# Performance work log

Measured on AMD Instinct MI355X. Metric: run time of the kernel, lower is better.

## Reference

```python
import jax, jax.numpy as jnp
import numpy as np

B, S, D_MODEL, D_ATTN = 4, 2048, 1024, 1024
NEG_INF = jnp.float32(-jnp.inf)


def setup_inputs() -> dict:
    key = jax.random.key(0)
    ks = jax.random.split(key, 6)
    scale = 1.0 / np.sqrt(D_MODEL)
    return {
        "x": jax.random.normal(ks[0], (B, S, D_MODEL), dtype=jnp.float32),
        "mask": jnp.ones((B, S), dtype=jnp.float32),
        "Wq": jax.random.normal(ks[1], (D_ATTN, D_MODEL), dtype=jnp.float32) * scale,
        "Wk": jax.random.normal(ks[2], (D_ATTN, D_MODEL), dtype=jnp.float32) * scale,
        "Wv": jax.random.normal(ks[3], (D_ATTN, D_MODEL), dtype=jnp.float32) * scale,
        "Wo": jax.random.normal(ks[4], (D_MODEL, D_ATTN), dtype=jnp.float32) * scale,
        "bo": jnp.zeros((D_MODEL,), dtype=jnp.float32),
    }


def reference(x, mask, Wq, Wk, Wv, Wo, bo):
    # x: [B,S,Dm]; torch Linear weight is [out,in], so y = x @ W.T
    q = jnp.einsum("bsd,ad->bsa", x, Wq)  # [B,S,Da]
    k = jnp.einsum("bsd,ad->bsa", x, Wk)
    v = jnp.einsum("bsd,ad->bsa", x, Wv)  # NOTE: v from x (original quirk)
    logits = jnp.einsum("bqa,bka->bqk", q, k)  # [B,S,S]
    # causal mask (cross_attention=True path): keep lower triangle incl. diag
    causal = jnp.tril(jnp.ones((S, S), dtype=bool))
    logits = jnp.where(causal[None], logits, NEG_INF)
    # padding mask: outer product of per-token mask
    square_mask = mask[:, :, None] * mask[:, None, :]  # [B,S,S]
    logits = jnp.where(square_mask == 1, logits, NEG_INF)
    # scale by sqrt(d_model) AFTER masking (as in original)
    attn = jax.nn.softmax(logits / jnp.sqrt(jnp.float32(D_MODEL)), axis=-1)
    attn_out = jnp.einsum("bqk,bka->bqa", attn, v)  # [B,S,Da]
    return jnp.einsum("bsa,da->bsd", attn_out, Wo) + bo
```

## Files before the change

### kernel.cpp

```cpp
#include <hip/hip_runtime.h>
#include <hip/hip_bf16.h>
#include <cstdio>

typedef __bf16 bf16x8 __attribute__((ext_vector_type(8)));
typedef float f32x4 __attribute__((ext_vector_type(4)));

#define BM 128
#define BN 128
#define BK 64

__device__ __forceinline__ unsigned short f2bf(float f) {
  union { float f; unsigned u; } v; v.f = f;
  unsigned u = v.u;
  return (unsigned short)((u + 0x7FFFu + ((u >> 16) & 1u)) >> 16);
}

__device__ __forceinline__ float bf2f(unsigned short s) {
  union { unsigned u; float f; } v; v.u = ((unsigned)s) << 16;
  return v.f;
}

#define GLOAD16(gsrc, ldst) \
  __builtin_amdgcn_global_load_lds((const __attribute__((address_space(1))) void*)(gsrc), \
                                   (__attribute__((address_space(3))) void*)(ldst), 16, 0, 0)

template<int EPI>
__global__ __launch_bounds__(256, 2)
void gemm_bt(const unsigned short* __restrict__ A, const unsigned short* __restrict__ B,
             void* __restrict__ Cv, void* __restrict__ Cv2, const float* __restrict__ bias,
             int K, int ldA, int ldB, int ldC,
             long aBat, long bBat, long cBat,
             int causalSkip, int causalKlim, float scale, int revM)
{
  const int by = revM ? (gridDim.y - 1 - blockIdx.y) : blockIdx.y;
  const int m0 = by * BM;
  const int n0 = blockIdx.x * BN;
  if (causalSkip && n0 > m0) return;
  const int bz = blockIdx.z;

  const unsigned short* Ab = A + (long)bz * aBat + (long)m0 * ldA;
  const unsigned short* Bb = B + (long)bz * bBat + (long)n0 * ldB;

  __shared__ short lds[2][2][BM * BK];

  const int tid = threadIdx.x;
  const int lane = tid & 63;
  const int wave = tid >> 6;
  const int wr = wave >> 1, wc = wave & 1;

  const int Keff = causalKlim ? min(K, m0 + BM) : K;
  const int nk = Keff / BK;

  const int srow = tid >> 3;
  const int sch = tid & 7;

  const f32x4 fzero = {0.f, 0.f, 0.f, 0.f};
  f32x4 acc[4][4];
#pragma unroll
  for (int i = 0; i < 4; i++)
#pragma unroll
    for (int j = 0; j < 4; j++) acc[i][j] = fzero;

  int aOff[4][2], bOff[4][2];
#pragma unroll
  for (int i = 0; i < 4; i++) {
#pragma unroll
    for (int s = 0; s < 2; s++) {
      int ra = wr * 64 + i * 16 + (lane & 15);
      aOff[i][s] = ra * BK + (((s * 4 + (lane >> 4)) ^ (ra & 7)) * 8);
      int rb = wc * 64 + i * 16 + (lane & 15);
      bOff[i][s] = rb * BK + (((s * 4 + (lane >> 4)) ^ (rb & 7)) * 8);
    }
  }

  auto stage = [&](int buf, int kt) {
    const unsigned short* Ak = Ab + kt * BK;
    const unsigned short* Bk = Bb + kt * BK;
#pragma unroll
    for (int r = 0; r < 4; r++) {
      int row = r * 32 + srow;
      int sc = sch ^ (row & 7);
      GLOAD16(Ak + (long)row * ldA + sc * 8, &lds[buf][0][(r * 32 + wave * 8) * BK]);
    }
#pragma unroll
    for (int r = 0; r < 4; r++) {
      int row = r * 32 + srow;
      int sc = sch ^ (row & 7);
      GLOAD16(Bk + (long)row * ldB + sc * 8, &lds[buf][1][(r * 32 + wave * 8) * BK]);
    }
  };

  stage(0, 0);
  __syncthreads();

  int cur = 0;
  for (int kt = 0; kt < nk; kt++) {
    if (kt + 1 < nk) stage(cur ^ 1, kt + 1);
    const short* La = lds[cur][0];
    const short* Lb = lds[cur][1];
#pragma unroll
    for (int s = 0; s < 2; s++) {
      bf16x8 av[4], bv[4];
#pragma unroll
      for (int i = 0; i < 4; i++) av[i] = *reinterpret_cast<const bf16x8*>(La + aOff[i][s]);
#pragma unroll
      for (int j = 0; j < 4; j++) bv[j] = *reinterpret_cast<const bf16x8*>(Lb + bOff[j][s]);
#pragma unroll
      for (int i = 0; i < 4; i++)
#pragma unroll
        for (int j = 0; j < 4; j++)
          acc[i][j] = __builtin_amdgcn_mfma_f32_16x16x32_bf16(av[i], bv[j], acc[i][j], 0, 0, 0);
    }
    __syncthreads();
    cur ^= 1;
  }

  const int rb4 = (lane >> 4) * 4;
  const int cl = lane & 15;
#pragma unroll
  for (int i = 0; i < 4; i++) {
#pragma unroll
    for (int j = 0; j < 4; j++) {
      const int gm = m0 + wr * 64 + i * 16 + rb4;
      const int gn = n0 + wc * 64 + j * 16 + cl;
      if (EPI == 0) {
        unsigned short* C = (unsigned short*)Cv + (long)bz * cBat;
#pragma unroll
        for (int r = 0; r < 4; r++)
          C[(long)(gm + r) * ldC + gn] = f2bf(acc[i][j][r] * scale);
      } else if (EPI == 2) {
        float* C = (float*)Cv;
        const float bb = bias[gn];
#pragma unroll
        for (int r = 0; r < 4; r++)
          C[(long)(gm + r) * ldC + gn] = acc[i][j][r] + bb;
      } else if (EPI == 4) {
        if (gn < 2048) {
          unsigned short* C = (unsigned short*)Cv;
#pragma unroll
          for (int r = 0; r < 4; r++)
            C[(long)(gm + r) * ldC + gn] = f2bf(acc[i][j][r]);
        } else {
          const int d = gn - 2048;
          const int b = gm >> 11;
          const int sIdx = gm & 2047;
          unsigned short* C = (unsigned short*)Cv2 + (long)b * (2048L * 1024)
                              + (long)d * 2048 + sIdx;
          ushort4 pk;
          pk.x = f2bf(acc[i][j][0]);
          pk.y = f2bf(acc[i][j][1]);
          pk.z = f2bf(acc[i][j][2]);
          pk.w = f2bf(acc[i][j][3]);
          *reinterpret_cast<ushort4*>(C) = pk;
        }
      }
    }
  }
}

__global__ __launch_bounds__(256)
void softmax_rows(const unsigned short* __restrict__ Sb, const float* __restrict__ maskv,
                  unsigned short* __restrict__ P, int Sdim)
{
  const int q = blockIdx.x;
  const int b = blockIdx.y;
  const int kmax = (q & ~127) + 128;
  const unsigned short* row = Sb + ((long)b * Sdim + q) * Sdim;
  unsigned short* prow = P + ((long)b * Sdim + q) * Sdim;
  const float* mrow = maskv + (long)b * Sdim;
  const int tid = threadIdx.x;
  const float mq = mrow[q];
  const int k0 = tid * 8;
  const bool live = (k0 < kmax);

  float v[8];
  if (live) {
    uint4 raw = *reinterpret_cast<const uint4*>(row + k0);
    const unsigned short* us = reinterpret_cast<const unsigned short*>(&raw);
    float4 ma = *reinterpret_cast<const float4*>(mrow + k0);
    float4 mb = *reinterpret_cast<const float4*>(mrow + k0 + 4);
    float mv[8] = {ma.x, ma.y, ma.z, ma.w, mb.x, mb.y, mb.z, mb.w};
#pragma unroll
    for (int u = 0; u < 8; u++) {
      const int k = k0 + u;
      const bool ok = (k <= q) && (mq * mv[u] == 1.0f);
      v[u] = ok ? bf2f(us[u]) : -INFINITY;
    }
  } else {
#pragma unroll
    for (int u = 0; u < 8; u++) v[u] = -INFINITY;
  }

  float mx = -INFINITY;
#pragma unroll
  for (int u = 0; u < 8; u++) mx = fmaxf(mx, v[u]);
#pragma unroll
  for (int o = 32; o; o >>= 1) mx = fmaxf(mx, __shfl_xor(mx, o));
  __shared__ float redm[4], reds[4];
  if ((tid & 63) == 0) redm[tid >> 6] = mx;
  __syncthreads();
  mx = fmaxf(fmaxf(redm[0], redm[1]), fmaxf(redm[2], redm[3]));

  float p[8];
  float sm = 0.f;
#pragma unroll
  for (int u = 0; u < 8; u++) {
    p[u] = (v[u] > -INFINITY) ? __expf(v[u] - mx) : 0.f;
    sm += p[u];
  }
#pragma unroll
  for (int o = 32; o; o >>= 1) sm += __shfl_xor(sm, o);
  if ((tid & 63) == 0) reds[tid >> 6] = sm;
  __syncthreads();
  sm = reds[0] + reds[1] + reds[2] + reds[3];
  const float inv = 1.0f / sm;

  if (live) {
    union { unsigned short us[8]; uint4 u4; } pk;
#pragma unroll
    for (int u = 0; u < 8; u++) pk.us[u] = f2bf(p[u] * inv);
    *reinterpret_cast<uint4*>(prow + k0) = pk.u4;
  }
}

__global__ __launch_bounds__(256)
void cast_f32_bf16(const float* __restrict__ in, unsigned short* __restrict__ out, int n)
{
  const int i = (blockIdx.x * 256 + threadIdx.x) * 8;
  if (i >= n) return;
  float4 a = *reinterpret_cast<const float4*>(in + i);
  float4 b = *reinterpret_cast<const float4*>(in + i + 4);
  union { unsigned short us[8]; uint4 u4; } pk;
  pk.us[0] = f2bf(a.x); pk.us[1] = f2bf(a.y); pk.us[2] = f2bf(a.z); pk.us[3] = f2bf(a.w);
  pk.us[4] = f2bf(b.x); pk.us[5] = f2bf(b.y); pk.us[6] = f2bf(b.z); pk.us[7] = f2bf(b.w);
  *reinterpret_cast<uint4*>(out + i) = pk.u4;
}

__global__ __launch_bounds__(256)
void cast_weights(const float* __restrict__ w0, const float* __restrict__ w1,
                  const float* __restrict__ w2, const float* __restrict__ w3,
                  unsigned short* __restrict__ dqkv, unsigned short* __restrict__ dout)
{
  const int z = blockIdx.z;
  const float* src = (z == 0) ? w0 : (z == 1) ? w1 : (z == 2) ? w2 : w3;
  unsigned short* dst = (z < 3) ? (dqkv + (long)z * 1024 * 1024) : dout;
  const int i = (blockIdx.x * 256 + threadIdx.x) * 8;
  float4 a = *reinterpret_cast<const float4*>(src + i);
  float4 b = *reinterpret_cast<const float4*>(src + i + 4);
  union { unsigned short us[8]; uint4 u4; } pk;
  pk.us[0] = f2bf(a.x); pk.us[1] = f2bf(a.y); pk.us[2] = f2bf(a.z); pk.us[3] = f2bf(a.w);
  pk.us[4] = f2bf(b.x); pk.us[5] = f2bf(b.y); pk.us[6] = f2bf(b.z); pk.us[7] = f2bf(b.w);
  *reinterpret_cast<uint4*>(dst + i) = pk.u4;
}

extern "C" void kernel_launch(void* const* d_in, const int* in_sizes, int n_in,
                              void* d_out, int out_size, void* d_ws, size_t ws_size,
                              hipStream_t stream)
{
  const int B = 4, S = 2048, D = 1024;
  const float* x  = (const float*)d_in[0];
  const float* mk = (const float*)d_in[1];
  const float* Wq = (const float*)d_in[2];
  const float* Wk = (const float*)d_in[3];
  const float* Wv = (const float*)d_in[4];
  const float* Wo = (const float*)d_in[5];
  const float* bo = (const float*)d_in[6];
  float* out = (float*)d_out;

  char* ws = (char*)d_ws;
  const long MB = 1024L * 1024L;
  unsigned short* Xbf  = (unsigned short*)(ws + 0);
  unsigned short* QKb  = (unsigned short*)(ws + 16 * MB);
  unsigned short* Vt   = (unsigned short*)(ws + 48 * MB);
  unsigned short* Wqkv = (unsigned short*)(ws + 64 * MB);
  unsigned short* Wob  = (unsigned short*)(ws + 70 * MB);
  unsigned short* Sbuf = (unsigned short*)(ws + 72 * MB);
  unsigned short* P    = QKb;
  unsigned short* O    = Xbf;

  if (ws_size < (size_t)(104 * MB)) {
    fprintf(stderr, "kernel_launch: ws too small (%zu bytes, need 104MB)\n", ws_size);
    return;
  }

  cast_f32_bf16<<<dim3((B * S * D) / 8 / 256), 256, 0, stream>>>(x, Xbf, B * S * D);
  cast_weights<<<dim3((D * D) / 8 / 256, 1, 4), 256, 0, stream>>>(Wq, Wk, Wv, Wo, Wqkv, Wob);

  const dim3 blk(256);
  dim3 gQKV(3072 / BN, 8192 / BM, 1);
  gemm_bt<4><<<gQKV, blk, 0, stream>>>(Xbf, Wqkv, QKb, Vt, nullptr,
                                       1024, 1024, 1024, 2048,
                                       0, 0, 0, 0, 0, 1.0f, 0);
  dim3 gS(2048 / BN, 2048 / BM, 4);
  gemm_bt<0><<<gS, blk, 0, stream>>>(QKb, QKb + 1024, Sbuf, nullptr, nullptr,
                                     1024, 2048, 2048, 2048,
                                     (long)S * 2048, (long)S * 2048, (long)S * S,
                                     1, 0, 0.03125f, 0);
  softmax_rows<<<dim3(2048, 4), blk, 0, stream>>>(Sbuf, mk, P, 2048);
  dim3 gO(1024 / BN, 2048 / BM, 4);
  gemm_bt<0><<<gO, blk, 0, stream>>>(P, Vt, O, nullptr, nullptr,
                                     2048, 2048, 2048, 1024,
                                     (long)S * S, (long)D * S, (long)S * D,
                                     0, 1, 1.0f, 1);
  dim3 gF(1024 / BN, 8192 / BM, 1);
  gemm_bt<2><<<gF, blk, 0, stream>>>(O, Wob, out, nullptr, bo,
                                     1024, 1024, 1024, 1024,
                                     0, 0, 0, 0, 0, 1.0f, 0);
}
```

Measured before the change: 185.9 us.

## Single-buffer GEMM LDS, raise occupancy, add XCD block swizzle, split Q/K outputs

The GEMM now uses a single LDS buffer instead of double buffering, which halves shared memory, and raises the launch-bounds occupancy hint from 2 to 3 blocks. Block indices are remapped so that consecutive tiles land on the same XCD for better L2 reuse. Q and K are written to separate contiguous buffers instead of one interleaved one, and the two cast kernels are merged into one launch. The cost is that global loads are no longer overlapped with MFMA work within a block, so latency hiding now relies on more resident blocks.

After: 183.0 us. About the same (-1.6%).

```diff
diff --git a/kernel.cpp b/kernel.cpp
--- a/kernel.cpp
+++ b/kernel.cpp
@@ -25,23 +25,33 @@
                                    (__attribute__((address_space(3))) void*)(ldst), 16, 0, 0)
 
 template<int EPI>
-__global__ __launch_bounds__(256, 2)
+__global__ __launch_bounds__(256, 3)
 void gemm_bt(const unsigned short* __restrict__ A, const unsigned short* __restrict__ B,
-             void* __restrict__ Cv, void* __restrict__ Cv2, const float* __restrict__ bias,
+             void* __restrict__ Cv, void* __restrict__ Cv2, void* __restrict__ Cv3,
+             const float* __restrict__ bias,
              int K, int ldA, int ldB, int ldC,
              long aBat, long bBat, long cBat,
              int causalSkip, int causalKlim, float scale, int revM)
 {
-  const int by = revM ? (gridDim.y - 1 - blockIdx.y) : blockIdx.y;
+  const int gx = gridDim.x;
+  const int nwg = gx * gridDim.y;
+  const int flat = blockIdx.y * gx + blockIdx.x;
+  const int qch = nwg >> 3, rch = nwg & 7;
+  const int xcd = flat & 7, idx = flat >> 3;
+  const int swz = (xcd < rch ? xcd * (qch + 1) : rch * (qch + 1) + (xcd - rch) * qch) + idx;
+  const int bx = swz % gx;
+  int by = swz / gx;
+  if (revM) by = gridDim.y - 1 - by;
+
   const int m0 = by * BM;
-  const int n0 = blockIdx.x * BN;
+  const int n0 = bx * BN;
   if (causalSkip && n0 > m0) return;
   const int bz = blockIdx.z;
 
   const unsigned short* Ab = A + (long)bz * aBat + (long)m0 * ldA;
   const unsigned short* Bb = B + (long)bz * bBat + (long)n0 * ldB;
 
-  __shared__ short lds[2][2][BM * BK];
+  __shared__ short lds[2][BM * BK];
 
   const int tid = threadIdx.x;
   const int lane = tid & 63;
@@ -73,38 +83,30 @@
     }
   }
 
-  auto stage = [&](int buf, int kt) {
+  for (int kt = 0; kt < nk; kt++) {
     const unsigned short* Ak = Ab + kt * BK;
     const unsigned short* Bk = Bb + kt * BK;
 #pragma unroll
     for (int r = 0; r < 4; r++) {
       int row = r * 32 + srow;
       int sc = sch ^ (row & 7);
-      GLOAD16(Ak + (long)row * ldA + sc * 8, &lds[buf][0][(r * 32 + wave * 8) * BK]);
+      GLOAD16(Ak + (long)row * ldA + sc * 8, &lds[0][(r * 32 + wave * 8) * BK]);
     }
 #pragma unroll
     for (int r = 0; r < 4; r++) {
       int row = r * 32 + srow;
       int sc = sch ^ (row & 7);
-      GLOAD16(Bk + (long)row * ldB + sc * 8, &lds[buf][1][(r * 32 + wave * 8) * BK]);
-    }
-  };
-
-  stage(0, 0);
-  __syncthreads();
-
-  int cur = 0;
-  for (int kt = 0; kt < nk; kt++) {
-    if (kt + 1 < nk) stage(cur ^ 1, kt + 1);
-    const short* La = lds[cur][0];
-    const short* Lb = lds[cur][1];
+      GLOAD16(Bk + (long)row * ldB + sc * 8, &lds[1][(r * 32 + wave * 8) * BK]);
+    }
+    __syncthreads();
+
 #pragma unroll
     for (int s = 0; s < 2; s++) {
       bf16x8 av[4], bv[4];
 #pragma unroll
-      for (int i = 0; i < 4; i++) av[i] = *reinterpret_cast<const bf16x8*>(La + aOff[i][s]);
-#pragma unroll
-      for (int j = 0; j < 4; j++) bv[j] = *reinterpret_cast<const bf16x8*>(Lb + bOff[j][s]);
+      for (int i = 0; i < 4; i++) av[i] = *reinterpret_cast<const bf16x8*>(lds[0] + aOff[i][s]);
+#pragma unroll
+      for (int j = 0; j < 4; j++) bv[j] = *reinterpret_cast<const bf16x8*>(lds[1] + bOff[j][s]);
 #pragma unroll
       for (int i = 0; i < 4; i++)
 #pragma unroll
@@ -112,7 +114,6 @@
           acc[i][j] = __builtin_amdgcn_mfma_f32_16x16x32_bf16(av[i], bv[j], acc[i][j], 0, 0, 0);
     }
     __syncthreads();
-    cur ^= 1;
   }
 
   const int rb4 = (lane >> 4) * 4;
@@ -135,16 +136,21 @@
         for (int r = 0; r < 4; r++)
           C[(long)(gm + r) * ldC + gn] = acc[i][j][r] + bb;
       } else if (EPI == 4) {
-        if (gn < 2048) {
+        if (gn < 1024) {
           unsigned short* C = (unsigned short*)Cv;
 #pragma unroll
           for (int r = 0; r < 4; r++)
-            C[(long)(gm + r) * ldC + gn] = f2bf(acc[i][j][r]);
+            C[(long)(gm + r) * 1024 + gn] = f2bf(acc[i][j][r]);
+        } else if (gn < 2048) {
+          unsigned short* C = (unsigned short*)Cv2;
+#pragma unroll
+          for (int r = 0; r < 4; r++)
+            C[(long)(gm + r) * 1024 + (gn - 1024)] = f2bf(acc[i][j][r]);
         } else {
           const int d = gn - 2048;
           const int b = gm >> 11;
           const int sIdx = gm & 2047;
-          unsigned short* C = (unsigned short*)Cv2 + (long)b * (2048L * 1024)
+          unsigned short* C = (unsigned short*)Cv3 + (long)b * (2048L * 1024)
                               + (long)d * 2048 + sIdx;
           ushort4 pk;
           pk.x = f2bf(acc[i][j][0]);
@@ -224,27 +230,25 @@
 }
 
 __global__ __launch_bounds__(256)
-void cast_f32_bf16(const float* __restrict__ in, unsigned short* __restrict__ out, int n)
+void cast_all(const float* __restrict__ x, const float* __restrict__ w0,
+              const float* __restrict__ w1, const float* __restrict__ w2,
+              const float* __restrict__ w3,
+              unsigned short* __restrict__ xb, unsigned short* __restrict__ dqkv,
+              unsigned short* __restrict__ dout)
 {
-  const int i = (blockIdx.x * 256 + threadIdx.x) * 8;
-  if (i >= n) return;
-  float4 a = *reinterpret_cast<const float4*>(in + i);
-  float4 b = *reinterpret_cast<const float4*>(in + i + 4);
-  union { unsigned short us[8]; uint4 u4; } pk;
-  pk.us[0] = f2bf(a.x); pk.us[1] = f2bf(a.y); pk.us[2] = f2bf(a.z); pk.us[3] = f2bf(a.w);
-  pk.us[4] = f2bf(b.x); pk.us[5] = f2bf(b.y); pk.us[6] = f2bf(b.z); pk.us[7] = f2bf(b.w);
-  *reinterpret_cast<uint4*>(out + i) = pk.u4;
-}
-
-__global__ __launch_bounds__(256)
-void cast_weights(const float* __restrict__ w0, const float* __restrict__ w1,
-                  const float* __restrict__ w2, const float* __restrict__ w3,
-                  unsigned short* __restrict__ dqkv, unsigned short* __restrict__ dout)
-{
-  const int z = blockIdx.z;
-  const float* src = (z == 0) ? w0 : (z == 1) ? w1 : (z == 2) ? w2 : w3;
-  unsigned short* dst = (z < 3) ? (dqkv + (long)z * 1024 * 1024) : dout;
-  const int i = (blockIdx.x * 256 + threadIdx.x) * 8;
+  const int blk = blockIdx.x;
+  const float* src;
+  unsigned short* dst;
+  int i;
+  if (blk < 4096) {
+    src = x; dst = xb; i = (blk * 256 + threadIdx.x) * 8;
+  } else {
+    const int w = (blk - 4096) >> 9;
+    const int off = (blk - 4096) & 511;
+    src = (w == 0) ? w0 : (w == 1) ? w1 : (w == 2) ? w2 : w3;
+    dst = (w < 3) ? (dqkv + (long)w * 1024 * 1024) : dout;
+    i = (off * 256 + threadIdx.x) * 8;
+  }
   float4 a = *reinterpret_cast<const float4*>(src + i);
   float4 b = *reinterpret_cast<const float4*>(src + i + 4);
   union { unsigned short us[8]; uint4 u4; } pk;
@@ -270,12 +274,13 @@
   char* ws = (char*)d_ws;
   const long MB = 1024L * 1024L;
   unsigned short* Xbf  = (unsigned short*)(ws + 0);
-  unsigned short* QKb  = (unsigned short*)(ws + 16 * MB);
+  unsigned short* Qb   = (unsigned short*)(ws + 16 * MB);
+  unsigned short* Kb   = (unsigned short*)(ws + 32 * MB);
   unsigned short* Vt   = (unsigned short*)(ws + 48 * MB);
   unsigned short* Wqkv = (unsigned short*)(ws + 64 * MB);
   unsigned short* Wob  = (unsigned short*)(ws + 70 * MB);
   unsigned short* Sbuf = (unsigned short*)(ws + 72 * MB);
-  unsigned short* P    = QKb;
+  unsigned short* P    = Qb;
   unsigned short* O    = Xbf;
 
   if (ws_size < (size_t)(104 * MB)) {
@@ -283,27 +288,26 @@
     return;
   }
 
-  cast_f32_bf16<<<dim3((B * S * D) / 8 / 256), 256, 0, stream>>>(x, Xbf, B * S * D);
-  cast_weights<<<dim3((D * D) / 8 / 256, 1, 4), 256, 0, stream>>>(Wq, Wk, Wv, Wo, Wqkv, Wob);
+  cast_all<<<dim3(4096 + 2048), 256, 0, stream>>>(x, Wq, Wk, Wv, Wo, Xbf, Wqkv, Wob);
 
   const dim3 blk(256);
   dim3 gQKV(3072 / BN, 8192 / BM, 1);
-  gemm_bt<4><<<gQKV, blk, 0, stream>>>(Xbf, Wqkv, QKb, Vt, nullptr,
-                                       1024, 1024, 1024, 2048,
+  gemm_bt<4><<<gQKV, blk, 0, stream>>>(Xbf, Wqkv, Qb, Kb, Vt, nullptr,
+                                       1024, 1024, 1024, 0,
                                        0, 0, 0, 0, 0, 1.0f, 0);
   dim3 gS(2048 / BN, 2048 / BM, 4);
-  gemm_bt<0><<<gS, blk, 0, stream>>>(QKb, QKb + 1024, Sbuf, nullptr, nullptr,
-                                     1024, 2048, 2048, 2048,
-                                     (long)S * 2048, (long)S * 2048, (long)S * S,
+  gemm_bt<0><<<gS, blk, 0, stream>>>(Qb, Kb, Sbuf, nullptr, nullptr, nullptr,
+                                     1024, 1024, 1024, 2048,
+                                     (long)S * 1024, (long)S * 1024, (long)S * S,
                                      1, 0, 0.03125f, 0);
   softmax_rows<<<dim3(2048, 4), blk, 0, stream>>>(Sbuf, mk, P, 2048);
   dim3 gO(1024 / BN, 2048 / BM, 4);
-  gemm_bt<0><<<gO, blk, 0, stream>>>(P, Vt, O, nullptr, nullptr,
+  gemm_bt<0><<<gO, blk, 0, stream>>>(P, Vt, O, nullptr, nullptr, nullptr,
                                      2048, 2048, 2048, 1024,
                                      (long)S * S, (long)D * S, (long)S * D,
                                      0, 1, 1.0f, 1);
   dim3 gF(1024 / BN, 8192 / BM, 1);
-  gemm_bt<2><<<gF, blk, 0, stream>>>(O, Wob, out, nullptr, bo,
+  gemm_bt<2><<<gF, blk, 0, stream>>>(O, Wob, out, nullptr, nullptr, bo,
                                      1024, 1024, 1024, 1024,
                                      0, 0, 0, 0, 0, 1.0f, 0);
 }
```
